# Kernel optimization log

Measured on AMD Instinct MI355X. Metric: run time of the kernel, lower is better.

The kernel has to match this reference:

```python
import jax, jax.numpy as jnp
import numpy as np

B, M, C, D, FF, FEAT = 1, 1024, 128, 512, 1024, 20
PAIR = 3 * D + 2 * FEAT  # slow_scorer_size = 1576


def _ffnn(x, W0, b0, W1, b1):
    # FFNN(depth=1): hidden relu layer then linear output (eval mode, no dropout)
    return jax.nn.relu(x @ W0 + b0) @ W1 + b1


def _batch_gather(x, idx):
    # x: [B, M, ...], idx: [B, ...] int -> gather along mention dim per batch
    return jax.vmap(lambda xb, ib: xb[ib])(x, idx)


def _bucket_distance(d):
    # log-scale distance buckets 0..9 (identity for d<=4)
    log_idx = jnp.floor(jnp.log(jnp.maximum(d, 1).astype(jnp.float32)) / jnp.log(2.0)).astype(jnp.int32) + 3
    return jnp.clip(jnp.where(d <= 4, d, log_idx), 0, 9)


def setup_inputs() -> dict:
    key = jax.random.key(0)
    ks = jax.random.split(key, 10)
    s = 0.02
    return {
        'mention_emb': jax.random.normal(ks[0], (B, M, D), dtype=jnp.float32),
        'mention_cluster_ids': jax.random.randint(ks[1], (B, M), 0, 200),
        'mention_speaker_ids': jax.random.randint(ks[2], (B, M), 0, 2),
        'ms_W0': jax.random.normal(ks[3], (D, FF), dtype=jnp.float32) * s,
        'ms_b0': jnp.zeros((FF,), jnp.float32),
        'ms_W1': jax.random.normal(ks[4], (FF, 1), dtype=jnp.float32) * s,
        'ms_b1': jnp.zeros((1,), jnp.float32),
        'sp_W0': jax.random.normal(ks[5], (PAIR, FF), dtype=jnp.float32) * s,
        'sp_b0': jnp.zeros((FF,), jnp.float32),
        'sp_W1': jax.random.normal(ks[6], (FF, 1), dtype=jnp.float32) * s,
        'sp_b1': jnp.zeros((1,), jnp.float32),
        'speaker_emb': jax.random.normal(ks[7], (2, FEAT), dtype=jnp.float32) * s,
        'bucket_emb': jax.random.normal(ks[8], (10, FEAT), dtype=jnp.float32) * s,
    }


def reference(mention_emb, mention_cluster_ids, mention_speaker_ids,
              ms_W0, ms_b0, ms_W1, ms_b1,
              sp_W0, sp_b0, sp_W1, sp_b1,
              speaker_emb, bucket_emb):
    # mention scoring
    mention_scores = _ffnn(mention_emb, ms_W0, ms_b0, ms_W1, ms_b1)[..., 0]  # [B, M]

    # get_antecedent_info: fixed window of C previous mentions
    offsets = jnp.arange(1, C + 1)[None, None, :]                    # [1,1,C]
    raw = jnp.arange(M)[None, :, None] - offsets                      # [1,M,C]
    antecedents = jnp.broadcast_to(jnp.clip(raw, 0, M - 1), (B, M, C))
    ant_mask = jnp.broadcast_to(raw >= 0, (B, M, C))

    fast_scores = _batch_gather(mention_scores, antecedents) + mention_scores[:, :, None]
    antecedent_emb = _batch_gather(mention_emb, antecedents)          # [B,M,C,D]

    # slow pair scorer features
    same_speaker = (_batch_gather(mention_speaker_ids, antecedents) == mention_speaker_ids[:, :, None]).astype(jnp.int32)
    speaker_feat = speaker_emb[same_speaker]                          # [B,M,C,FEAT]
    bucket_feat = jnp.broadcast_to(bucket_emb[_bucket_distance(offsets)], (B, M, C, FEAT))

    src = jnp.broadcast_to(mention_emb[:, :, None, :], (B, M, C, D))
    pair_emb = jnp.concatenate([src, antecedent_emb, src * antecedent_emb, speaker_feat, bucket_feat], axis=-1)
    slow_scores = _ffnn(pair_emb, sp_W0, sp_b0, sp_W1, sp_b1)[..., 0]  # [B,M,C]

    antecedent_scores = fast_scores + slow_scores + jnp.log(ant_mask.astype(jnp.float32))
    overall_scores = jnp.concatenate([jnp.zeros((B, M, 1), jnp.float32), antecedent_scores], axis=2)
    overall_dist = jax.nn.softmax(overall_scores, axis=-1)
    eps = 1e-6
    overall_dist = jnp.clip(overall_dist, eps, 1.0 - eps)
    overall_dist = overall_dist / jnp.sum(overall_dist, axis=-1, keepdims=True)

    # coref loss from cluster ids
    ant_cluster = _batch_gather(mention_cluster_ids, antecedents) * ant_mask.astype(mention_cluster_ids.dtype)
    same_cluster = ant_cluster == mention_cluster_ids[:, :, None]
    non_dummy = (mention_cluster_ids > 0)[:, :, None]
    ant_labels = same_cluster & non_dummy
    dummy_labels = ~jnp.any(ant_labels, axis=2, keepdims=True)
    overall_labels = jnp.concatenate([dummy_labels, ant_labels], axis=2)
    loss = -jnp.sum(jnp.log(overall_dist) * overall_labels.astype(jnp.float32), axis=2)
    loss = jnp.mean(jnp.sum(loss, axis=1))
    return overall_dist, loss
```

## Files before the change

kernel.cpp:

```cpp
#include <hip/hip_runtime.h>
#include <math.h>

#define MM 1024
#define DD 512
#define CC 128
#define LDSR 516


typedef __attribute__((ext_vector_type(8))) short bf16x8;
typedef __attribute__((ext_vector_type(4), aligned(8))) short bf16x4a;
typedef __attribute__((ext_vector_type(4))) float f32x4;
typedef __attribute__((ext_vector_type(16))) float f32x16;

__device__ __forceinline__ ushort bf16_rn(float x) {
    uint u = __float_as_uint(x);
    uint r = u + 0x7fffu + ((u >> 16) & 1u);
    return (ushort)(r >> 16);
}
__device__ __forceinline__ float bf16_to_f(ushort u) {
    return __uint_as_float(((uint)u) << 16);
}
__device__ __forceinline__ bf16x8 ld_lds16(const ushort* p) {
    bf16x4a lo = *(const bf16x4a*)p;
    bf16x4a hi = *(const bf16x4a*)(p + 4);
    return __builtin_shufflevector(lo, hi, 0, 1, 2, 3, 4, 5, 6, 7);
}

__global__ __launch_bounds__(256) void prep_emb(const float* __restrict__ emb,
                                                ushort* __restrict__ embb)
{
    int i = blockIdx.x * 256 + threadIdx.x;
    float2 v = ((const float2*)emb)[i];
    ushort2 o;
    o.x = bf16_rn(v.x);
    o.y = bf16_rn(v.y);
    ((ushort2*)embb)[i] = o;
}

__global__ __launch_bounds__(256) void prep_wall(const float* __restrict__ ms_W0,
                                                 const float* __restrict__ sp_W0,
                                                 ushort* __restrict__ Wall)
{
    __shared__ float t[64][65];
    const int k0 = blockIdx.x * 64;
    const int n0 = blockIdx.y * 64;
    const int g = n0 >> 10;
    const float* src = (g == 0) ? ms_W0 : (sp_W0 + (size_t)(g - 1) * 512 * 1024);
    const int col0 = n0 & 1023;
    const int tr = threadIdx.x >> 6, tc = threadIdx.x & 63;
#pragma unroll
    for (int i = 0; i < 16; ++i) {
        int k = tr + i * 4;
        t[k][tc] = src[(size_t)(k0 + k) * 1024 + col0 + tc];
    }
    __syncthreads();
    const int f = threadIdx.x >> 2;
    const int c4 = threadIdx.x & 3;
    ushort tmp[16];
#pragma unroll
    for (int j = 0; j < 16; ++j) tmp[j] = bf16_rn(t[c4 * 16 + j][f]);
    uint4* dst = (uint4*)(Wall + (size_t)(n0 + f) * 512 + k0 + c4 * 16);
    dst[0] = *(uint4*)&tmp[0];
    dst[1] = *(uint4*)&tmp[8];
}

__global__ __launch_bounds__(64) void prep_wfrag(const float* __restrict__ sp_W0,
                                                 ushort* __restrict__ Wfrag)
{
    const int ts = blockIdx.x;
    const int l = threadIdx.x;
    const int tt = ts >> 5, s = ts & 31;
    const int f = tt * 32 + (l & 31);
    const int kb = s * 16 + (l >> 5) * 8;
    const float* W = sp_W0 + (size_t)1024 * 1024;
    ushort tmp[8];
#pragma unroll
    for (int j = 0; j < 8; ++j) tmp[j] = bf16_rn(W[(size_t)(kb + j) * 1024 + f]);
    uint4* dst = (uint4*)(Wfrag + ((size_t)ts * 64 + l) * 8);
    *dst = *(uint4*)&tmp[0];
}

__global__ __launch_bounds__(256) void gemm_h_mfma(
    const ushort* __restrict__ embb, const ushort* __restrict__ Wall,
    float* __restrict__ H)
{
    const int n0 = blockIdx.x * 128;
    const int m0 = blockIdx.y * 128;
    const int lane = threadIdx.x & 63, wave = threadIdx.x >> 6;
    const int wx = wave & 1, wy = wave >> 1;
    const int l15 = lane & 15, lq = lane >> 4;

    const ushort* arow[4];
#pragma unroll
    for (int mi = 0; mi < 4; ++mi)
        arow[mi] = embb + (size_t)(m0 + wy * 64 + mi * 16 + l15) * 512;
    const ushort* brow[4];
#pragma unroll
    for (int ni = 0; ni < 4; ++ni)
        brow[ni] = Wall + (size_t)(n0 + wx * 64 + ni * 16 + l15) * 512;

    f32x4 acc[4][4];
#pragma unroll
    for (int i = 0; i < 4; ++i)
#pragma unroll
        for (int j = 0; j < 4; ++j) acc[i][j] = (f32x4)0.f;

    for (int kt = 0; kt < 512; kt += 32) {
        const int ko = kt + lq * 8;
        bf16x8 av[4], bv[4];
#pragma unroll
        for (int mi = 0; mi < 4; ++mi) av[mi] = *(const bf16x8*)(arow[mi] + ko);
#pragma unroll
        for (int ni = 0; ni < 4; ++ni) bv[ni] = *(const bf16x8*)(brow[ni] + ko);
#pragma unroll
        for (int mi = 0; mi < 4; ++mi)
#pragma unroll
            for (int ni = 0; ni < 4; ++ni)
                acc[mi][ni] = __builtin_amdgcn_mfma_f32_16x16x32_bf16(av[mi], bv[ni], acc[mi][ni], 0, 0, 0);
    }
#pragma unroll
    for (int mi = 0; mi < 4; ++mi)
#pragma unroll
        for (int r = 0; r < 4; ++r) {
            int mrow = m0 + wy * 64 + mi * 16 + lq * 4 + r;
#pragma unroll
            for (int ni = 0; ni < 4; ++ni)
                H[(size_t)mrow * 3072 + n0 + wx * 64 + ni * 16 + l15] = acc[mi][ni][r];
        }
}

__global__ void small_proj(const float* __restrict__ speaker_emb,
                           const float* __restrict__ bucket_emb,
                           const float* __restrict__ sp_W0,
                           float* __restrict__ spk_proj, float* __restrict__ bkt_proj)
{
    int r = blockIdx.x;
    const float* e; const float* W; float* out;
    if (r < 2) { e = speaker_emb + r * 20; W = sp_W0 + (size_t)1536 * 1024; out = spk_proj + r * 1024; }
    else       { e = bucket_emb + (r - 2) * 20; W = sp_W0 + (size_t)1556 * 1024; out = bkt_proj + (r - 2) * 1024; }
    float ek[20];
#pragma unroll
    for (int k = 0; k < 20; ++k) ek[k] = e[k];
    for (int f = threadIdx.x; f < 1024; f += blockDim.x) {
        float s = 0.f;
#pragma unroll
        for (int k = 0; k < 20; ++k) s = fmaf(ek[k], W[(size_t)k * 1024 + f], s);
        out[f] = s;
    }
}

__global__ __launch_bounds__(256) void mention_score(
    const float* __restrict__ H, const float* __restrict__ ms_b0,
    const float* __restrict__ ms_W1, const float* __restrict__ ms_b1,
    float* __restrict__ ms)
{
    int m = blockIdx.x;
    float v = 0.f;
    for (int f = threadIdx.x; f < 1024; f += 256) {
        float h = H[(size_t)m * 3072 + f] + ms_b0[f];
        v += fmaxf(h, 0.f) * ms_W1[f];
    }
#pragma unroll
    for (int o = 1; o < 64; o <<= 1) v += __shfl_xor(v, o);
    __shared__ float sm[4];
    if ((threadIdx.x & 63) == 0) sm[threadIdx.x >> 6] = v;
    __syncthreads();
    if (threadIdx.x == 0) ms[m] = sm[0] + sm[1] + sm[2] + sm[3] + ms_b1[0];
}

__global__ __launch_bounds__(1024, 4) void pair_mfma(
    const ushort* __restrict__ embb, const ushort* __restrict__ Wfrag,
    const float* __restrict__ H, const float* __restrict__ spk_proj,
    const float* __restrict__ bkt_proj, const float* __restrict__ sp_b0,
    const float* __restrict__ sp_W1, const int* __restrict__ speaker,
    float* __restrict__ slow)
{
    extern __shared__ ushort Alds[];
    float* red = (float*)(Alds + 128 * LDSR);
    int* meta_ss = (int*)(red + 16 * 128);
    int* meta_bk = meta_ss + 128;
    const int m = blockIdx.x;
    const int tid = threadIdx.x;
    const int spk_m = speaker[m];

    {
        const int c = tid >> 3;
        const int kh = (tid & 7) * 64;
        int a = m - 1 - c; if (a < 0) a = 0;
        const ushort* ea = embb + (size_t)a * 512 + kh;
        const ushort* em = embb + (size_t)m * 512 + kh;
        ushort* dst = Alds + c * LDSR + kh;
#pragma unroll
        for (int j = 0; j < 64; j += 8) {
            bf16x8 va = *(const bf16x8*)(ea + j);
            bf16x8 vm = *(const bf16x8*)(em + j);
            uint pr[4];
#pragma unroll
            for (int p = 0; p < 4; ++p) {
                float q0 = bf16_to_f((ushort)va[2 * p])     * bf16_to_f((ushort)vm[2 * p]);
                float q1 = bf16_to_f((ushort)va[2 * p + 1]) * bf16_to_f((ushort)vm[2 * p + 1]);
                pr[p] = __builtin_amdgcn_perm(__float_as_uint(q1), __float_as_uint(q0), 0x07060302u);
            }
            *(uint2*)(dst + j)     = *(uint2*)&pr[0];
            *(uint2*)(dst + j + 4) = *(uint2*)&pr[2];
        }
        if ((tid & 7) == 0) {
            meta_ss[c] = (speaker[a] == spk_m) ? 1 : 0;
            int off = c + 1;
            int bk;
            if (off <= 4) bk = off;
            else { bk = 31 - __clz(off) + 3; if (bk > 9) bk = 9; }
            meta_bk[c] = bk;
        }
    }
    __syncthreads();

    const int lane = tid & 63;
    const int wave = __builtin_amdgcn_readfirstlane(tid >> 6);
    const int l31 = lane & 31, k5 = lane >> 5;
    const int f0 = wave * 64;

    const ushort* bb = Wfrag + (size_t)(wave * 2) * 16384 + (size_t)lane * 8;
    const ushort* ab = Alds + l31 * LDSR + k5 * 8;

    for (int pass = 0; pass < 2; ++pass) {
        const int c0 = pass * 64;
        const ushort* ap = ab + c0 * LDSR;
        f32x16 acc[2][2];
#pragma unroll
        for (int i = 0; i < 2; ++i)
#pragma unroll
            for (int j = 0; j < 2; ++j) acc[i][j] = (f32x16)0.f;

#pragma unroll 2
        for (int s = 0; s < 32; ++s) {
            bf16x8 b0 = *(const bf16x8*)(bb + s * 512);
            bf16x8 b1 = *(const bf16x8*)(bb + 16384 + s * 512);
            bf16x8 a0 = ld_lds16(ap + s * 16);
            bf16x8 a1 = ld_lds16(ap + 32 * LDSR + s * 16);
            acc[0][0] = __builtin_amdgcn_mfma_f32_32x32x16_bf16(a0, b0, acc[0][0], 0, 0, 0);
            acc[0][1] = __builtin_amdgcn_mfma_f32_32x32x16_bf16(a0, b1, acc[0][1], 0, 0, 0);
            acc[1][0] = __builtin_amdgcn_mfma_f32_32x32x16_bf16(a1, b0, acc[1][0], 0, 0, 0);
            acc[1][1] = __builtin_amdgcn_mfma_f32_32x32x16_bf16(a1, b1, acc[1][1], 0, 0, 0);
        }

        float srcb[2], w1v[2], sp0v[2], sp1v[2], bk9v[2];
#pragma unroll
        for (int ni = 0; ni < 2; ++ni) {
            int fcol = f0 + ni * 32 + l31;
            srcb[ni] = H[(size_t)m * 3072 + 1024 + fcol] + sp_b0[fcol];
            w1v[ni]  = sp_W1[fcol];
            sp0v[ni] = spk_proj[fcol];
            sp1v[ni] = spk_proj[1024 + fcol];
            bk9v[ni] = bkt_proj[9 * 1024 + fcol];
        }
#pragma unroll
        for (int mi = 0; mi < 2; ++mi) {
#pragma unroll
            for (int reg = 0; reg < 16; ++reg) {
                const int c = c0 + mi * 32 + 4 * k5 + (reg & 3) + 8 * (reg >> 2);
                int a = m - 1 - c; if (a < 0) a = 0;
                const int ss = meta_ss[c];
                const float* antp = H + (size_t)a * 3072 + 2048;
                float s = 0.f;
#pragma unroll
                for (int ni = 0; ni < 2; ++ni) {
                    const int fcol = f0 + ni * 32 + l31;
                    float bval = pass ? bk9v[ni] : bkt_proj[(size_t)meta_bk[c] * 1024 + fcol];
                    float pre = acc[mi][ni][reg] + srcb[ni] + antp[fcol] + (ss ? sp1v[ni] : sp0v[ni]) + bval;
                    s += fmaxf(pre, 0.f) * w1v[ni];
                }
                s += __shfl_xor(s, 1); s += __shfl_xor(s, 2); s += __shfl_xor(s, 4);
                s += __shfl_xor(s, 8); s += __shfl_xor(s, 16);
                if (l31 == 0) red[wave * 128 + c] = s;
            }
        }
    }
    __syncthreads();
    if (tid < 128) {
        float s = 0.f;
#pragma unroll
        for (int i = 0; i < 16; ++i) s += red[i * 128 + tid];
        slow[(size_t)m * 128 + tid] = s;
    }
}

__device__ __forceinline__ float bsum2(float v, float* sm) {
#pragma unroll
    for (int o = 1; o < 64; o <<= 1) v += __shfl_xor(v, o);
    __syncthreads();
    if ((threadIdx.x & 63) == 0) sm[threadIdx.x >> 6] = v;
    __syncthreads();
    return sm[0] + sm[1];
}
__device__ __forceinline__ float bmax2(float v, float* sm) {
#pragma unroll
    for (int o = 1; o < 64; o <<= 1) v = fmaxf(v, __shfl_xor(v, o));
    __syncthreads();
    if ((threadIdx.x & 63) == 0) sm[threadIdx.x >> 6] = v;
    __syncthreads();
    return fmaxf(sm[0], sm[1]);
}

__global__ __launch_bounds__(128) void softmax_loss(
    const float* __restrict__ slow, const float* __restrict__ ms,
    const float* __restrict__ sp_b1, const int* __restrict__ cluster,
    float* __restrict__ out, float* __restrict__ loss_partial)
{
    const int m = blockIdx.x, c = threadIdx.x;
    __shared__ float sm[2];
    const int raw = m - 1 - c;
    const bool maskv = raw >= 0;
    const int a = maskv ? raw : 0;
    float score = slow[(size_t)m * 128 + c] + sp_b1[0] + ms[m] + ms[a];
    if (!maskv) score = -INFINITY;

    float mx = fmaxf(bmax2(score, sm), 0.f);
    float e = expf(score - mx);
    float e0 = expf(0.f - mx);
    float sum = bsum2(e, sm) + e0;
    float p = e / sum, p0 = e0 / sum;
    const float eps = 1e-6f;
    p  = fminf(fmaxf(p,  eps), 1.f - eps);
    p0 = fminf(fmaxf(p0, eps), 1.f - eps);
    float sum2 = bsum2(p, sm) + p0;
    p /= sum2; p0 /= sum2;
    out[(size_t)m * 129 + 1 + c] = p;
    if (c == 0) out[(size_t)m * 129] = p0;

    const int cid = cluster[m];
    const bool lbl = maskv && (cid > 0) && (cluster[a] == cid);
    float anyc = bsum2(lbl ? 1.f : 0.f, sm);
    float lsum = bsum2(lbl ? -logf(p) : 0.f, sm);
    if (c == 0) {
        if (anyc == 0.f) lsum += -logf(p0);
        loss_partial[m] = lsum;
    }
}

__global__ void loss_sum(const float* __restrict__ lp, float* __restrict__ out) {
    float v = 0.f;
    for (int i = threadIdx.x; i < 1024; i += 256) v += lp[i];
#pragma unroll
    for (int o = 1; o < 64; o <<= 1) v += __shfl_xor(v, o);
    __shared__ float sm[4];
    if ((threadIdx.x & 63) == 0) sm[threadIdx.x >> 6] = v;
    __syncthreads();
    if (threadIdx.x == 0) out[(size_t)1024 * 129] = sm[0] + sm[1] + sm[2] + sm[3];
}

extern "C" void kernel_launch(void* const* d_in, const int* in_sizes, int n_in,
                              void* d_out, int out_size, void* d_ws, size_t ws_size,
                              hipStream_t stream)
{
    const float* emb   = (const float*)d_in[0];
    const int*   clus  = (const int*)  d_in[1];
    const int*   spk   = (const int*)  d_in[2];
    const float* ms_W0 = (const float*)d_in[3];
    const float* ms_b0 = (const float*)d_in[4];
    const float* ms_W1 = (const float*)d_in[5];
    const float* ms_b1 = (const float*)d_in[6];
    const float* sp_W0 = (const float*)d_in[7];
    const float* sp_b0 = (const float*)d_in[8];
    const float* sp_W1 = (const float*)d_in[9];
    const float* sp_b1 = (const float*)d_in[10];
    const float* spke  = (const float*)d_in[11];
    const float* bkte  = (const float*)d_in[12];

    float* ws = (float*)d_ws;
    float* H        = ws;
    float* slow     = ws + 3145728;
    float* spk_proj = ws + 3276800;
    float* bkt_proj = ws + 3278848;
    float* msc      = ws + 3289088;
    float* lossp    = ws + 3290112;
    ushort* embb    = (ushort*)(ws + 3291136);
    ushort* Wall    = (ushort*)(ws + 3553280);
    ushort* Wfrag   = Wall + (size_t)3072 * 512;
    float* out = (float*)d_out;

    const int pair_lds = 128 * LDSR * 2 + 16 * 128 * 4 + 256 * 4;

    static bool attr_set = false;
    if (!attr_set) {
        hipFuncSetAttribute((const void*)pair_mfma,
                            hipFuncAttributeMaxDynamicSharedMemorySize,
                            pair_lds);
        attr_set = true;
    }

    hipLaunchKernelGGL(prep_emb, dim3(1024), dim3(256), 0, stream, emb, embb);
    hipLaunchKernelGGL(prep_wall, dim3(8, 48), dim3(256), 0, stream, ms_W0, sp_W0, Wall);
    hipLaunchKernelGGL(prep_wfrag, dim3(1024), dim3(64), 0, stream, sp_W0, Wfrag);
    hipLaunchKernelGGL(gemm_h_mfma, dim3(24, 8), dim3(256), 0, stream, embb, Wall, H);
    hipLaunchKernelGGL(small_proj, dim3(12), dim3(256), 0, stream, spke, bkte, sp_W0, spk_proj, bkt_proj);
    hipLaunchKernelGGL(mention_score, dim3(1024), dim3(256), 0, stream, H, ms_b0, ms_W1, ms_b1, msc);
    hipLaunchKernelGGL(pair_mfma, dim3(1024), dim3(1024), pair_lds, stream,
                       embb, Wfrag, H, spk_proj, bkt_proj, sp_b0, sp_W1, spk, slow);
    hipLaunchKernelGGL(softmax_loss, dim3(1024), dim3(128), 0, stream,
                       slow, msc, sp_b1, clus, out, lossp);
    hipLaunchKernelGGL(loss_sum, dim3(1), dim3(256), 0, stream, lossp, out);
}
```

Measured before the change: 383.7 us.

## Split pair kernel over antecedent halves with 512-thread blocks

The pair scoring kernel now launches a 2D grid where each block handles 64 antecedents of one mention and loops over both halves of the hidden dimension. Before, one 1024-thread block covered all 128 antecedents. Blocks become smaller with less LDS, so more can be resident per CU, and partial sums accumulate in LDS across the two passes. It also raises wave priority around the MFMA group. The trade-off is that the weight fragments are streamed twice per mention, once per block, and there is an extra barrier per pass.

```diff
diff --git a/kernel.cpp b/kernel.cpp
--- a/kernel.cpp
+++ b/kernel.cpp
@@ -168,7 +168,7 @@
     if (threadIdx.x == 0) ms[m] = sm[0] + sm[1] + sm[2] + sm[3] + ms_b1[0];
 }
 
-__global__ __launch_bounds__(1024, 4) void pair_mfma(
+__global__ __launch_bounds__(512, 4) void pair_mfma(
     const ushort* __restrict__ embb, const ushort* __restrict__ Wfrag,
     const float* __restrict__ H, const float* __restrict__ spk_proj,
     const float* __restrict__ bkt_proj, const float* __restrict__ sp_b0,
@@ -176,17 +176,18 @@
     float* __restrict__ slow)
 {
     extern __shared__ ushort Alds[];
-    float* red = (float*)(Alds + 128 * LDSR);
-    int* meta_ss = (int*)(red + 16 * 128);
-    int* meta_bk = meta_ss + 128;
+    float* red = (float*)(Alds + 64 * LDSR);
+    int* meta_ss = (int*)(red + 8 * 64);
+    int* meta_bk = meta_ss + 64;
     const int m = blockIdx.x;
+    const int cbase = blockIdx.y * 64;
     const int tid = threadIdx.x;
     const int spk_m = speaker[m];
 
     {
         const int c = tid >> 3;
         const int kh = (tid & 7) * 64;
-        int a = m - 1 - c; if (a < 0) a = 0;
+        int a = m - 1 - (cbase + c); if (a < 0) a = 0;
         const ushort* ea = embb + (size_t)a * 512 + kh;
         const ushort* em = embb + (size_t)m * 512 + kh;
         ushort* dst = Alds + c * LDSR + kh;
@@ -206,7 +207,7 @@
         }
         if ((tid & 7) == 0) {
             meta_ss[c] = (speaker[a] == spk_m) ? 1 : 0;
-            int off = c + 1;
+            int off = cbase + c + 1;
             int bk;
             if (off <= 4) bk = off;
             else { bk = 31 - __clz(off) + 3; if (bk > 9) bk = 9; }
@@ -218,14 +219,12 @@
     const int lane = tid & 63;
     const int wave = __builtin_amdgcn_readfirstlane(tid >> 6);
     const int l31 = lane & 31, k5 = lane >> 5;
-    const int f0 = wave * 64;
-
-    const ushort* bb = Wfrag + (size_t)(wave * 2) * 16384 + (size_t)lane * 8;
+
     const ushort* ab = Alds + l31 * LDSR + k5 * 8;
 
     for (int pass = 0; pass < 2; ++pass) {
-        const int c0 = pass * 64;
-        const ushort* ap = ab + c0 * LDSR;
+        const int f0 = pass * 512 + wave * 64;
+        const ushort* bb = Wfrag + (size_t)(pass * 16 + wave * 2) * 16384 + (size_t)lane * 8;
         f32x16 acc[2][2];
 #pragma unroll
         for (int i = 0; i < 2; ++i)
@@ -236,12 +235,14 @@
         for (int s = 0; s < 32; ++s) {
             bf16x8 b0 = *(const bf16x8*)(bb + s * 512);
             bf16x8 b1 = *(const bf16x8*)(bb + 16384 + s * 512);
-            bf16x8 a0 = ld_lds16(ap + s * 16);
-            bf16x8 a1 = ld_lds16(ap + 32 * LDSR + s * 16);
+            bf16x8 a0 = ld_lds16(ab + s * 16);
+            bf16x8 a1 = ld_lds16(ab + 32 * LDSR + s * 16);
+            __builtin_amdgcn_s_setprio(1);
             acc[0][0] = __builtin_amdgcn_mfma_f32_32x32x16_bf16(a0, b0, acc[0][0], 0, 0, 0);
             acc[0][1] = __builtin_amdgcn_mfma_f32_32x32x16_bf16(a0, b1, acc[0][1], 0, 0, 0);
             acc[1][0] = __builtin_amdgcn_mfma_f32_32x32x16_bf16(a1, b0, acc[1][0], 0, 0, 0);
             acc[1][1] = __builtin_amdgcn_mfma_f32_32x32x16_bf16(a1, b1, acc[1][1], 0, 0, 0);
+            __builtin_amdgcn_s_setprio(0);
         }
 
         float srcb[2], w1v[2], sp0v[2], sp1v[2], bk9v[2];
@@ -258,30 +259,33 @@
         for (int mi = 0; mi < 2; ++mi) {
 #pragma unroll
             for (int reg = 0; reg < 16; ++reg) {
-                const int c = c0 + mi * 32 + 4 * k5 + (reg & 3) + 8 * (reg >> 2);
-                int a = m - 1 - c; if (a < 0) a = 0;
+                const int c = mi * 32 + 4 * k5 + (reg & 3) + 8 * (reg >> 2);
+                int a = m - 1 - (cbase + c); if (a < 0) a = 0;
                 const int ss = meta_ss[c];
                 const float* antp = H + (size_t)a * 3072 + 2048;
                 float s = 0.f;
 #pragma unroll
                 for (int ni = 0; ni < 2; ++ni) {
                     const int fcol = f0 + ni * 32 + l31;
-                    float bval = pass ? bk9v[ni] : bkt_proj[(size_t)meta_bk[c] * 1024 + fcol];
+                    float bval = cbase ? bk9v[ni] : bkt_proj[(size_t)meta_bk[c] * 1024 + fcol];
                     float pre = acc[mi][ni][reg] + srcb[ni] + antp[fcol] + (ss ? sp1v[ni] : sp0v[ni]) + bval;
                     s += fmaxf(pre, 0.f) * w1v[ni];
                 }
                 s += __shfl_xor(s, 1); s += __shfl_xor(s, 2); s += __shfl_xor(s, 4);
                 s += __shfl_xor(s, 8); s += __shfl_xor(s, 16);
-                if (l31 == 0) red[wave * 128 + c] = s;
+                if (l31 == 0) {
+                    if (pass == 0) red[wave * 64 + c] = s;
+                    else           red[wave * 64 + c] += s;
+                }
             }
         }
-    }
-    __syncthreads();
-    if (tid < 128) {
+        __syncthreads();
+    }
+    if (tid < 64) {
         float s = 0.f;
 #pragma unroll
-        for (int i = 0; i < 16; ++i) s += red[i * 128 + tid];
-        slow[(size_t)m * 128 + tid] = s;
+        for (int i = 0; i < 8; ++i) s += red[i * 64 + tid];
+        slow[(size_t)m * 128 + cbase + tid] = s;
     }
 }
 
@@ -379,7 +383,7 @@
     ushort* Wfrag   = Wall + (size_t)3072 * 512;
     float* out = (float*)d_out;
 
-    const int pair_lds = 128 * LDSR * 2 + 16 * 128 * 4 + 256 * 4;
+    const int pair_lds = 64 * LDSR * 2 + 8 * 64 * 4 + 2 * 64 * 4;
 
     static bool attr_set = false;
     if (!attr_set) {
@@ -395,7 +399,7 @@
     hipLaunchKernelGGL(gemm_h_mfma, dim3(24, 8), dim3(256), 0, stream, embb, Wall, H);
     hipLaunchKernelGGL(small_proj, dim3(12), dim3(256), 0, stream, spke, bkte, sp_W0, spk_proj, bkt_proj);
     hipLaunchKernelGGL(mention_score, dim3(1024), dim3(256), 0, stream, H, ms_b0, ms_W1, ms_b1, msc);
-    hipLaunchKernelGGL(pair_mfma, dim3(1024), dim3(1024), pair_lds, stream,
+    hipLaunchKernelGGL(pair_mfma, dim3(1024, 2), dim3(512), pair_lds, stream,
                        embb, Wfrag, H, spk_proj, bkt_proj, sp_b0, sp_W1, spk, slow);
     hipLaunchKernelGGL(softmax_loss, dim3(1024), dim3(128), 0, stream,
                        slow, msc, sp_b1, clus, out, lossp);
```

Result: slower. 635.9 us (+65.7%).
